# Kernel optimization log

Hardware: AMD Instinct MI355X
Metric: run time of the kernel (lower is better)

The kernel has to match this reference:

```python
import jax, jax.numpy as jnp
import numpy as np

NUM_FIELDS = 24
FIELD_DIM = 2000
VOCAB = NUM_FIELDS * FIELD_DIM  # sum(field_dims) = 48000
EMBED_DIM = 64
H1, H2 = 64, 32
NUM_INTERACTIONS = 16
BATCH = 4096


def setup_inputs() -> dict:
    key = jax.random.key(0)
    ks = jax.random.split(key, 12)
    s = 0.05  # xavier-ish scale
    return {
        "x": jax.random.randint(ks[0], (BATCH, NUM_FIELDS), 0, FIELD_DIM, dtype=jnp.int32),
        # per-field embedding tables stacked: (num_fields, vocab, embed_dim)
        "tables": jax.random.normal(ks[1], (NUM_FIELDS, VOCAB, EMBED_DIM), jnp.float32) * s,
        "fc_w": jax.random.normal(ks[2], (VOCAB, 1), jnp.float32) * s,
        "fc_b": jnp.zeros((1,), jnp.float32),
        "w1": jax.random.normal(ks[3], (2 * EMBED_DIM, H1), jnp.float32) * s,
        "b1": jnp.zeros((H1,), jnp.float32),
        "w2": jax.random.normal(ks[4], (H1, H2), jnp.float32) * s,
        "b2": jnp.zeros((H2,), jnp.float32),
        "w3": jax.random.normal(ks[5], (H2, 1), jnp.float32) * s,
        "b3": jnp.zeros((1,), jnp.float32),
        "proj_w": jax.random.normal(ks[6], (EMBED_DIM, 1), jnp.float32) * s,
        "proj_b": jnp.zeros((1,), jnp.float32),
        "bias": jnp.zeros((1,), jnp.float32),
    }


def reference(x, tables, fc_w, fc_b, w1, b1, w2, b2, w3, b3, proj_w, proj_b, bias):
    offsets = jnp.arange(NUM_FIELDS, dtype=x.dtype) * FIELD_DIM  # cumsum of equal field_dims
    idx = x + offsets[None, :]  # (B, F)

    # FeaturesLinear: first-order term, (B, 1)
    linear_part = fc_w[idx].sum(axis=1) + fc_b

    # FeaturesEmbedding: per-field table lookup -> (B, F, D)
    emb = tables[jnp.arange(NUM_FIELDS)[None, :], idx]

    # FeatureInteractionDetector: all i<j pairs, concat, score with MLP
    iu, ju = jnp.triu_indices(NUM_FIELDS, k=1)  # (P,), P = F*(F-1)/2
    pair_emb = jnp.concatenate([emb[:, iu], emb[:, ju]], axis=-1)  # (B, P, 2D)
    h = jax.nn.relu(pair_emb @ w1 + b1)
    h = jax.nn.relu(h @ w2 + b2)
    scores = (h @ w3 + b3)[..., 0]  # (B, P)

    # topk over batch-mean scores, gather per-sample scores and pair indices
    _, top = jax.lax.top_k(scores.mean(axis=0), NUM_INTERACTIONS)  # (K,)
    sel_scores = scores[:, top]  # (B, K)
    sel_i, sel_j = iu[top], ju[top]

    # FeatureCrossing: elementwise product of selected pairs, score-weighted sum, project
    crossed = emb[:, sel_i] * emb[:, sel_j]  # (B, K, D)
    summed = jnp.sum(crossed * sel_scores[..., None], axis=1)  # (B, D)
    crossed_part = summed @ proj_w + proj_b  # (B, 1)

    out = linear_part + crossed_part + bias  # (B, 1)
    return out[:, 0]
```

## Files before the change

kernel.cpp:

```cpp
#include <hip/hip_runtime.h>
#include <stdint.h>

#define NF 24
#define FD 2000
#define VOCABSZ 48000
#define ED 64
#define H1D 64
#define H2D 32
#define NPAIR 276
#define BATCH 4096
#define NSEL 16
#define NTILE 256
#define PBASE 49152

typedef _Float16 f16x8 __attribute__((ext_vector_type(8)));
typedef _Float16 f16x2 __attribute__((ext_vector_type(2)));
typedef float f32x4 __attribute__((ext_vector_type(4)));

union U4 { f16x8 v; uint32_t u[4]; uint4 q; };
union H2U { f16x2 h; uint32_t u; };

__device__ __forceinline__ uint32_t pkrtz(float lo, float hi){
  uint32_t r; asm("v_cvt_pkrtz_f16_f32 %0, %1, %2" : "=v"(r) : "v"(lo), "v"(hi)); return r;
}
__device__ __forceinline__ uint32_t pk_add(uint32_t a, uint32_t b){
  uint32_t r; asm("v_pk_add_f16 %0, %1, %2" : "=v"(r) : "v"(a), "v"(b)); return r;
}
__device__ __forceinline__ uint32_t pk_mul(uint32_t a, uint32_t b){
  uint32_t r; asm("v_pk_mul_f16 %0, %1, %2" : "=v"(r) : "v"(a), "v"(b)); return r;
}
__device__ __forceinline__ uint32_t pk_relu(uint32_t a){
  uint32_t r; asm("v_pk_max_f16 %0, %1, %2" : "=v"(r) : "v"(a), "v"(0u)); return r;
}
__device__ __forceinline__ float fdot2(uint32_t a, uint32_t b, float c){
  H2U ua, ub; ua.u = a; ub.u = b;
  return __builtin_amdgcn_fdot2(ua.h, ub.h, c, false);
}
#define DPP_ADD(v, ctrl) \
  (v) += __int_as_float(__builtin_amdgcn_update_dpp(0, __float_as_int(v), (ctrl), 0xF, 0xF, true))

__device__ __forceinline__ float rowsum4(float v){
  float a = v, b;
  asm volatile("v_mov_b32 %0, %1" : "=v"(b) : "v"(a));
  asm volatile("v_permlane16_swap_b32 %0, %1" : "+v"(a), "+v"(b));
  a = a + b;
  asm volatile("v_mov_b32 %0, %1" : "=v"(b) : "v"(a));
  asm volatile("v_permlane32_swap_b32 %0, %1" : "+v"(a), "+v"(b));
  return a + b;
}

__global__ __launch_bounds__(1024) void k_pair(
    const int* __restrict__ x, const float* __restrict__ tables,
    const float* __restrict__ w1, const float* __restrict__ b1,
    const float* __restrict__ w2, const float* __restrict__ b2,
    const float* __restrict__ w3, const float* __restrict__ b3,
    const float* __restrict__ proj_w,
    float* __restrict__ sgT, float* __restrict__ part){
  __shared__ __align__(16) char smem[147456];
  const int tid  = threadIdx.x;
  const int bt   = blockIdx.x;
  const int lane = tid & 63;
  const int w    = tid >> 6;
  const int n    = lane & 15;
  const int kg   = lane >> 4;

  const int half = w >> 3;
  const int oq   = (w >> 1) & 3;
  const int fg   = w & 1;
  const int isPt = (half == 0);
  const float b3v = b3[0];

  const int o = 16*oq + n;
  U4 wp0, wp1;
  {
    const float* wsrc = w1 + (size_t)(isPt ? 0 : ED)*H1D + o;
    #pragma unroll
    for(int j=0;j<8;j++) wp0.v[j] = (_Float16)wsrc[(kg*8+j)*H1D];
    #pragma unroll
    for(int j=0;j<8;j++) wp1.v[j] = (_Float16)wsrc[(32+kg*8+j)*H1D];
  }
  const float b1v = isPt ? b1[o] : 0.f;

  U4 wf[2][2];
  #pragma unroll
  for(int kh=0;kh<2;kh++)
    #pragma unroll
    for(int nh=0;nh<2;nh++)
      #pragma unroll
      for(int q2=0;q2<4;q2++){
        float lo = w2[(kg*8 + 2*q2     + 32*kh)*H2D + n + 16*nh];
        float hi = w2[(kg*8 + 2*q2 + 1 + 32*kh)*H2D + n + 16*nh];
        wf[kh][nh].u[q2] = pkrtz(lo, hi);
      }
  float b2r[2][4], w3r[2][4];
  #pragma unroll
  for(int oh=0;oh<2;oh++)
    #pragma unroll
    for(int r=0;r<4;r++){
      b2r[oh][r] = b2[16*oh + kg*4 + r];
      w3r[oh][r] = w3[16*oh + kg*4 + r];
    }

  uint32_t pw2[8];
  #pragma unroll
  for(int j=0;j<8;j++) pw2[j] = pkrtz(proj_w[kg*16 + 2*j], proj_w[kg*16 + 2*j + 1]);

  #pragma unroll
  for(int i=0;i<3;i++){
    int c = i*1024 + tid;
    int rid = c >> 3;
    int qc = c & 7;
    int f = rid >> 4, b = rid & 15;
    int xv = x[(bt*16 + b)*NF + f];
    const float4* rp = (const float4*)(tables + ((size_t)f*VOCABSZ + (size_t)f*FD + (size_t)xv)*ED + qc*8);
    float4 v0 = rp[0], v1 = rp[1];
    uint4 pk;
    pk.x = pkrtz(v0.x, v0.y); pk.y = pkrtz(v0.z, v0.w);
    pk.z = pkrtz(v1.x, v1.y); pk.w = pkrtz(v1.z, v1.w);
    uint32_t db = ((uint32_t)(f*2048 + b*128 + qc*16)) ^ ((uint32_t)(b&7)<<4);
    *(uint4*)(smem + db) = pk;
  }
  __syncthreads();

  {
    const uint32_t rswz = ((uint32_t)(n&7))<<4;
    const int slab0 = isPt ? 0 : 24;
    for(int ff=0; ff<12; ff++){
      int f = fg*12 + ff;
      U4 a0, a1;
      a0.q = *(const uint4*)(smem + (((uint32_t)(f*2048 + n*128      + kg*16)) ^ rswz));
      a1.q = *(const uint4*)(smem + (((uint32_t)(f*2048 + n*128 + 64 + kg*16)) ^ rswz));
      f32x4 acc = {b1v, b1v, b1v, b1v};
      acc = __builtin_amdgcn_mfma_f32_16x16x32_f16(a0.v, wp0.v, acc, 0,0,0);
      acc = __builtin_amdgcn_mfma_f32_16x16x32_f16(a1.v, wp1.v, acc, 0,0,0);
      int sl = slab0 + f;
      #pragma unroll
      for(int r=0;r<4;r++){
        int bo = kg*4 + r;
        uint32_t db = ((uint32_t)(PBASE + sl*2048 + bo*128 + o*2)) ^ (((uint32_t)(bo&7))<<4);
        *(_Float16*)(smem + db) = (_Float16)acc[r];
      }
    }
  }
  __syncthreads();

  {
    int p0, np;
    if(w < 4){ np = 18; p0 = w*18; } else { np = 17; p0 = 72 + (w-4)*17; }
    int ii = 0, rem = p0;
    while(rem >= (NF-1-ii)){ rem -= (NF-1-ii); ii++; }
    int jj = ii + 1 + rem;

    const uint32_t aswz = ((uint32_t)(n&7))<<4;
    const uint32_t rowoff = (uint32_t)n*128;
    const uint32_t qoff = (uint32_t)kg*16;
    const uint32_t kg32 = (uint32_t)kg*32;

    int cached_i = -1;
    U4 ta0, ta1, ei0, ei1;

    for(int t=0;t<np;t++){
      int p = p0 + t;
      if(ii != cached_i){
        uint32_t tb = (uint32_t)(PBASE + ii*2048) + rowoff;
        ta0.q = *(const uint4*)(smem + ((tb + qoff     ) ^ aswz));
        ta1.q = *(const uint4*)(smem + ((tb + qoff + 64) ^ aswz));
        uint32_t ebi = (uint32_t)(ii*2048) + rowoff + kg32;
        ei0.q = *(const uint4*)(smem + ((ebi     ) ^ aswz));
        ei1.q = *(const uint4*)(smem + ((ebi + 16) ^ aswz));
        cached_i = ii;
      }
      uint32_t ub = (uint32_t)(PBASE + (24+jj)*2048) + rowoff;
      uint4 c0 = *(const uint4*)(smem + ((ub + qoff     ) ^ aswz));
      uint4 c1 = *(const uint4*)(smem + ((ub + qoff + 64) ^ aswz));
      uint32_t ebj = (uint32_t)(jj*2048) + rowoff + kg32;
      U4 ej0, ej1;
      ej0.q = *(const uint4*)(smem + ((ebj     ) ^ aswz));
      ej1.q = *(const uint4*)(smem + ((ebj + 16) ^ aswz));

      U4 h0, h1;
      h0.u[0]=pk_relu(pk_add(ta0.u[0],c0.x)); h0.u[1]=pk_relu(pk_add(ta0.u[1],c0.y));
      h0.u[2]=pk_relu(pk_add(ta0.u[2],c0.z)); h0.u[3]=pk_relu(pk_add(ta0.u[3],c0.w));
      h1.u[0]=pk_relu(pk_add(ta1.u[0],c1.x)); h1.u[1]=pk_relu(pk_add(ta1.u[1],c1.y));
      h1.u[2]=pk_relu(pk_add(ta1.u[2],c1.z)); h1.u[3]=pk_relu(pk_add(ta1.u[3],c1.w));

      f32x4 acc0 = {0.f,0.f,0.f,0.f}, acc1 = {0.f,0.f,0.f,0.f};
      acc0 = __builtin_amdgcn_mfma_f32_16x16x32_f16(wf[0][0].v, h0.v, acc0, 0,0,0);
      acc0 = __builtin_amdgcn_mfma_f32_16x16x32_f16(wf[1][0].v, h1.v, acc0, 0,0,0);
      acc1 = __builtin_amdgcn_mfma_f32_16x16x32_f16(wf[0][1].v, h0.v, acc1, 0,0,0);
      acc1 = __builtin_amdgcn_mfma_f32_16x16x32_f16(wf[1][1].v, h1.v, acc1, 0,0,0);

      float gp = 0.f;
      #pragma unroll
      for(int q=0;q<4;q++) gp = fdot2(pk_mul(ei0.u[q], ej0.u[q]), pw2[q],   gp);
      #pragma unroll
      for(int q=0;q<4;q++) gp = fdot2(pk_mul(ei1.u[q], ej1.u[q]), pw2[4+q], gp);
      gp = rowsum4(gp);

      float tsum = 0.f;
      #pragma unroll
      for(int r=0;r<4;r++){
        float v0 = acc0[r] + b2r[0][r]; v0 = v0>0.f?v0:0.f;
        float v1 = acc1[r] + b2r[1][r]; v1 = v1>0.f?v1:0.f;
        tsum += v0*w3r[0][r] + v1*w3r[1][r];
      }
      tsum = rowsum4(tsum);
      float sc = tsum + b3v;

      if(lane < 16) sgT[(size_t)bt*(NPAIR*16) + p*16 + lane] = sc * gp;

      float d = sc;
      DPP_ADD(d, 0x111);
      DPP_ADD(d, 0x112);
      DPP_ADD(d, 0x114);
      DPP_ADD(d, 0x118);
      if(lane == 15) part[(size_t)p*NTILE + bt] = d;

      if(++jj == NF){ ii++; jj = ii+1; }
    }
  }
}

__global__ __launch_bounds__(1024) void k_final(
    const int* __restrict__ x, const float* __restrict__ sgT,
    const float* __restrict__ part,
    const float* __restrict__ fc_w, const float* __restrict__ fc_b,
    const float* __restrict__ proj_b, const float* __restrict__ bias,
    float* __restrict__ out){
  __shared__ float means[NPAIR];
  __shared__ int sel[NSEL];
  int tid = threadIdx.x;
  int bt = blockIdx.x;

  {
    int p = tid >> 2, q = tid & 3;
    const float4* pp = (const float4*)(part + (size_t)p*NTILE + q*64);
    float4 s4 = {0.f,0.f,0.f,0.f};
    #pragma unroll
    for(int i=0;i<16;i++){
      float4 v = pp[i];
      s4.x += v.x; s4.y += v.y; s4.z += v.z; s4.w += v.w;
    }
    float s = (s4.x + s4.y) + (s4.z + s4.w);
    s += __shfl_xor(s, 1, 64);
    s += __shfl_xor(s, 2, 64);
    if(q == 0 && p < 256) means[p] = s;
    if(tid < 80){
      int p2 = 256 + (tid >> 2);
      const float4* pp2 = (const float4*)(part + (size_t)p2*NTILE + q*64);
      float4 t4 = {0.f,0.f,0.f,0.f};
      #pragma unroll
      for(int i=0;i<16;i++){
        float4 v = pp2[i];
        t4.x += v.x; t4.y += v.y; t4.z += v.z; t4.w += v.w;
      }
      float s2 = (t4.x + t4.y) + (t4.z + t4.w);
      s2 += __shfl_xor(s2, 1, 64);
      s2 += __shfl_xor(s2, 2, 64);
      if(q == 0) means[p2] = s2;
    }
  }
  __syncthreads();
  if(tid < 64){
    int l = tid;
    float v[5];
    #pragma unroll
    for(int q=0;q<5;q++){
      int i = l + q*64;
      v[q] = (i < NPAIR) ? means[i] : -3.0e38f;
    }
    for(int s=0;s<NSEL;s++){
      float bv = v[0]; int bslot = 0;
      #pragma unroll
      for(int q=1;q<5;q++){ if(v[q] > bv){ bv = v[q]; bslot = q; } }
      int bi = l + bslot*64;
      float cv = bv; int ci = bi;
      #pragma unroll
      for(int m=1;m<64;m<<=1){
        float ov = __shfl_xor(cv, m, 64);
        int   oi = __shfl_xor(ci, m, 64);
        if(ov > cv || (ov == cv && oi < ci)){ cv = ov; ci = oi; }
      }
      if(l == 0) sel[s] = ci;
      if(bi == ci) v[bslot] = -3.0e38f;
    }
  }
  __syncthreads();

  int row = tid >> 6, lane = tid & 63;
  int brow = bt*16 + row;
  float v = 0.f;
  if(lane < NSEL){
    v = sgT[(size_t)bt*(NPAIR*16) + sel[lane]*16 + row];
  } else if(lane >= 32 && lane < 32+NF){
    int fl = lane - 32;
    v = fc_w[x[brow*NF + fl] + fl*FD];
  }
  #pragma unroll
  for(int m=1;m<64;m<<=1) v += __shfl_xor(v, m, 64);
  if(lane == 0) out[brow] = v + fc_b[0] + proj_b[0] + bias[0];
}

extern "C" void kernel_launch(void* const* d_in, const int* in_sizes, int n_in,
                              void* d_out, int out_size, void* d_ws, size_t ws_size,
                              hipStream_t stream){
  const int*   x      = (const int*)  d_in[0];
  const float* tables = (const float*)d_in[1];
  const float* fc_w   = (const float*)d_in[2];
  const float* fc_b   = (const float*)d_in[3];
  const float* w1     = (const float*)d_in[4];
  const float* b1     = (const float*)d_in[5];
  const float* w2     = (const float*)d_in[6];
  const float* b2     = (const float*)d_in[7];
  const float* w3     = (const float*)d_in[8];
  const float* b3     = (const float*)d_in[9];
  const float* proj_w = (const float*)d_in[10];
  const float* proj_b = (const float*)d_in[11];
  const float* bias   = (const float*)d_in[12];
  float* out = (float*)d_out;

  float* sgT  = (float*)d_ws;
  float* part = sgT + (size_t)NTILE*NPAIR*16;

  k_pair<<<NTILE, 1024, 0, stream>>>(x, tables, w1, b1, w2, b2, w3, b3, proj_w, sgT, part);
  k_final<<<NTILE, 1024, 0, stream>>>(x, sgT, part, fc_w, fc_b, proj_b, bias, out);
}
```

Measured before the change: 48.81 us.

## Fuse pair-scoring and final kernels with grid-wide last-block top-k handoff

Merges the two kernels into one. Each block keeps its per-sample gated scores in LDS as fp16 instead of writing them to global memory. An atomic counter picks the last block to finish, which reduces the batch means and runs the top-k, then publishes the selection through a flag that the other blocks spin-wait on. This removes one kernel launch and the global round-trip of the score buffer, at the cost of a spin barrier that needs all 256 blocks resident at once, an extra memset, and fp16 rounding of the stored scores.

Measured after the change: 63.58 us. 30.2% more time.

```diff
diff --git a/kernel.cpp b/kernel.cpp
--- a/kernel.cpp
+++ b/kernel.cpp
@@ -12,6 +12,10 @@
 #define NSEL 16
 #define NTILE 256
 #define PBASE 49152
+#define SGB   147456
+#define MEANB 156288
+#define SELB  157392
+#define OLDB  157456
 
 typedef _Float16 f16x8 __attribute__((ext_vector_type(8)));
 typedef _Float16 f16x2 __attribute__((ext_vector_type(2)));
@@ -49,14 +53,22 @@
   return a + b;
 }
 
-__global__ __launch_bounds__(1024) void k_pair(
+__global__ __launch_bounds__(1024) void k_all(
     const int* __restrict__ x, const float* __restrict__ tables,
     const float* __restrict__ w1, const float* __restrict__ b1,
     const float* __restrict__ w2, const float* __restrict__ b2,
     const float* __restrict__ w3, const float* __restrict__ b3,
-    const float* __restrict__ proj_w,
-    float* __restrict__ sgT, float* __restrict__ part){
-  __shared__ __align__(16) char smem[147456];
+    const float* __restrict__ proj_w, const float* __restrict__ fc_w,
+    const float* __restrict__ fc_b, const float* __restrict__ proj_b,
+    const float* __restrict__ bias,
+    float* __restrict__ part, int* __restrict__ selg,
+    int* __restrict__ cnt, int* __restrict__ flag,
+    float* __restrict__ out){
+  __shared__ __align__(16) char smem[157472];
+  float* means_lds = (float*)(smem + MEANB);
+  int*   sel_lds   = (int*)(smem + SELB);
+  int*   old_lds   = (int*)(smem + OLDB);
+
   const int tid  = threadIdx.x;
   const int bt   = blockIdx.x;
   const int lane = tid & 63;
@@ -69,6 +81,7 @@
   const int fg   = w & 1;
   const int isPt = (half == 0);
   const float b3v = b3[0];
+  const float fcb = fc_b[0], pjb = proj_b[0], bsv = bias[0];
 
   const int o = 16*oq + n;
   U4 wp0, wp1;
@@ -207,7 +220,7 @@
       tsum = rowsum4(tsum);
       float sc = tsum + b3v;
 
-      if(lane < 16) sgT[(size_t)bt*(NPAIR*16) + p*16 + lane] = sc * gp;
+      if(lane < 16) *(_Float16*)(smem + SGB + p*32 + lane*2) = (_Float16)(sc * gp);
 
       float d = sc;
       DPP_ADD(d, 0x111);
@@ -219,86 +232,96 @@
       if(++jj == NF){ ii++; jj = ii+1; }
     }
   }
-}
-
-__global__ __launch_bounds__(1024) void k_final(
-    const int* __restrict__ x, const float* __restrict__ sgT,
-    const float* __restrict__ part,
-    const float* __restrict__ fc_w, const float* __restrict__ fc_b,
-    const float* __restrict__ proj_b, const float* __restrict__ bias,
-    float* __restrict__ out){
-  __shared__ float means[NPAIR];
-  __shared__ int sel[NSEL];
-  int tid = threadIdx.x;
-  int bt = blockIdx.x;
+  __syncthreads();
+
+  if(tid == 0)
+    old_lds[0] = __hip_atomic_fetch_add(cnt, 1, __ATOMIC_ACQ_REL, __HIP_MEMORY_SCOPE_AGENT);
+  __syncthreads();
+
+  if(old_lds[0] == NTILE-1){
+    {
+      int p = tid >> 2, q = tid & 3;
+      const float4* pp = (const float4*)(part + (size_t)p*NTILE + q*64);
+      float4 s4 = {0.f,0.f,0.f,0.f};
+      #pragma unroll
+      for(int i=0;i<16;i++){
+        float4 v = pp[i];
+        s4.x += v.x; s4.y += v.y; s4.z += v.z; s4.w += v.w;
+      }
+      float s = (s4.x + s4.y) + (s4.z + s4.w);
+      s += __shfl_xor(s, 1, 64);
+      s += __shfl_xor(s, 2, 64);
+      if(q == 0 && p < 256) means_lds[p] = s;
+      if(tid < 80){
+        int p2 = 256 + (tid >> 2);
+        const float4* pp2 = (const float4*)(part + (size_t)p2*NTILE + q*64);
+        float4 t4 = {0.f,0.f,0.f,0.f};
+        #pragma unroll
+        for(int i=0;i<16;i++){
+          float4 v = pp2[i];
+          t4.x += v.x; t4.y += v.y; t4.z += v.z; t4.w += v.w;
+        }
+        float s2 = (t4.x + t4.y) + (t4.z + t4.w);
+        s2 += __shfl_xor(s2, 1, 64);
+        s2 += __shfl_xor(s2, 2, 64);
+        if(q == 0) means_lds[p2] = s2;
+      }
+    }
+    __syncthreads();
+    if(tid < 64){
+      int l = tid;
+      float v[5];
+      #pragma unroll
+      for(int q=0;q<5;q++){
+        int i = l + q*64;
+        v[q] = (i < NPAIR) ? means_lds[i] : -3.0e38f;
+      }
+      for(int s=0;s<NSEL;s++){
+        float bv = v[0]; int bslot = 0;
+        #pragma unroll
+        for(int q=1;q<5;q++){ if(v[q] > bv){ bv = v[q]; bslot = q; } }
+        int bi = l + bslot*64;
+        float cv = bv; int ci = bi;
+        #pragma unroll
+        for(int m=1;m<64;m<<=1){
+          float ov = __shfl_xor(cv, m, 64);
+          int   oi = __shfl_xor(ci, m, 64);
+          if(ov > cv || (ov == cv && oi < ci)){ cv = ov; ci = oi; }
+        }
+        if(l == 0) sel_lds[s] = ci;
+        if(bi == ci) v[bslot] = -3.0e38f;
+      }
+    }
+    __syncthreads();
+    if(tid < NSEL) selg[tid] = sel_lds[tid];
+    __syncthreads();
+    if(tid == 0)
+      __hip_atomic_store(flag, 1, __ATOMIC_RELEASE, __HIP_MEMORY_SCOPE_AGENT);
+  } else {
+    if(tid == 0){
+      while(__hip_atomic_load(flag, __ATOMIC_RELAXED, __HIP_MEMORY_SCOPE_AGENT) == 0)
+        __builtin_amdgcn_s_sleep(8);
+      (void)__hip_atomic_load(flag, __ATOMIC_ACQUIRE, __HIP_MEMORY_SCOPE_AGENT);
+    }
+    __syncthreads();
+    if(tid < NSEL) sel_lds[tid] = selg[tid];
+    __syncthreads();
+  }
 
   {
-    int p = tid >> 2, q = tid & 3;
-    const float4* pp = (const float4*)(part + (size_t)p*NTILE + q*64);
-    float4 s4 = {0.f,0.f,0.f,0.f};
-    #pragma unroll
-    for(int i=0;i<16;i++){
-      float4 v = pp[i];
-      s4.x += v.x; s4.y += v.y; s4.z += v.z; s4.w += v.w;
-    }
-    float s = (s4.x + s4.y) + (s4.z + s4.w);
-    s += __shfl_xor(s, 1, 64);
-    s += __shfl_xor(s, 2, 64);
-    if(q == 0 && p < 256) means[p] = s;
-    if(tid < 80){
-      int p2 = 256 + (tid >> 2);
-      const float4* pp2 = (const float4*)(part + (size_t)p2*NTILE + q*64);
-      float4 t4 = {0.f,0.f,0.f,0.f};
-      #pragma unroll
-      for(int i=0;i<16;i++){
-        float4 v = pp2[i];
-        t4.x += v.x; t4.y += v.y; t4.z += v.z; t4.w += v.w;
-      }
-      float s2 = (t4.x + t4.y) + (t4.z + t4.w);
-      s2 += __shfl_xor(s2, 1, 64);
-      s2 += __shfl_xor(s2, 2, 64);
-      if(q == 0) means[p2] = s2;
-    }
-  }
-  __syncthreads();
-  if(tid < 64){
-    int l = tid;
-    float v[5];
-    #pragma unroll
-    for(int q=0;q<5;q++){
-      int i = l + q*64;
-      v[q] = (i < NPAIR) ? means[i] : -3.0e38f;
-    }
-    for(int s=0;s<NSEL;s++){
-      float bv = v[0]; int bslot = 0;
-      #pragma unroll
-      for(int q=1;q<5;q++){ if(v[q] > bv){ bv = v[q]; bslot = q; } }
-      int bi = l + bslot*64;
-      float cv = bv; int ci = bi;
-      #pragma unroll
-      for(int m=1;m<64;m<<=1){
-        float ov = __shfl_xor(cv, m, 64);
-        int   oi = __shfl_xor(ci, m, 64);
-        if(ov > cv || (ov == cv && oi < ci)){ cv = ov; ci = oi; }
-      }
-      if(l == 0) sel[s] = ci;
-      if(bi == ci) v[bslot] = -3.0e38f;
-    }
-  }
-  __syncthreads();
-
-  int row = tid >> 6, lane = tid & 63;
-  int brow = bt*16 + row;
-  float v = 0.f;
-  if(lane < NSEL){
-    v = sgT[(size_t)bt*(NPAIR*16) + sel[lane]*16 + row];
-  } else if(lane >= 32 && lane < 32+NF){
-    int fl = lane - 32;
-    v = fc_w[x[brow*NF + fl] + fl*FD];
-  }
-  #pragma unroll
-  for(int m=1;m<64;m<<=1) v += __shfl_xor(v, m, 64);
-  if(lane == 0) out[brow] = v + fc_b[0] + proj_b[0] + bias[0];
+    int row = w;
+    int brow = bt*16 + row;
+    float v = 0.f;
+    if(lane < NSEL){
+      v = (float)(*(const _Float16*)(smem + SGB + sel_lds[lane]*32 + row*2));
+    } else if(lane >= 32 && lane < 32+NF){
+      int fl = lane - 32;
+      v = fc_w[x[brow*NF + fl] + fl*FD];
+    }
+    #pragma unroll
+    for(int m=1;m<64;m<<=1) v += __shfl_xor(v, m, 64);
+    if(lane == 0) out[brow] = v + fcb + pjb + bsv;
+  }
 }
 
 extern "C" void kernel_launch(void* const* d_in, const int* in_sizes, int n_in,
@@ -319,9 +342,12 @@
   const float* bias   = (const float*)d_in[12];
   float* out = (float*)d_out;
 
-  float* sgT  = (float*)d_ws;
-  float* part = sgT + (size_t)NTILE*NPAIR*16;
-
-  k_pair<<<NTILE, 1024, 0, stream>>>(x, tables, w1, b1, w2, b2, w3, b3, proj_w, sgT, part);
-  k_final<<<NTILE, 1024, 0, stream>>>(x, sgT, part, fc_w, fc_b, proj_b, bias, out);
-}
+  float* part = (float*)d_ws;
+  int*   selg = (int*)(part + (size_t)NPAIR*NTILE);
+  int*   ctrl = selg + 16;
+
+  hipMemsetAsync(ctrl, 0, 8, stream);
+  k_all<<<NTILE, 1024, 0, stream>>>(x, tables, w1, b1, w2, b2, w3, b3,
+                                    proj_w, fc_w, fc_b, proj_b, bias,
+                                    part, selg, ctrl, ctrl+1, out);
+}
```
